# Kernel tuning notes

Hardware: AMD Instinct MI355X
Metric: run time of the kernel (lower is better)

The kernel has to match this reference:

```python
import jax, jax.numpy as jnp
import numpy as np

KSIZE = 3
PAD = (KSIZE - 1) // 2
SIGMA = 0.15 * KSIZE + 0.35  # 0.8, used for BOTH spatial and range weights (as in source)


def gaussian_kernel(ksize, sigma):
    if sigma <= 0:
        sigma = 0.3 * ((ksize - 1) * 0.5 - 1) + 0.8
    xs = np.arange(ksize, dtype=np.float32) - ksize // 2
    k1 = np.exp(-xs ** 2 / (2.0 * sigma ** 2))
    k = k1[:, None] * k1[None, :]
    return jnp.asarray((k / k.sum()).astype(np.float32))


def setup_inputs() -> dict:
    key = jax.random.key(0)
    ks = jax.random.split(key, 5)
    B, C_in, H, W = 8, 256, 128, 128
    C2 = 128
    x1 = jax.random.normal(ks[0], (B, C_in, H, W), jnp.float32)
    x2 = jax.random.normal(ks[1], (B, C2, 2 * H, 2 * W), jnp.float32)
    # Conv2d(in_ch, 1, kernel_size=1): weight [out=1, in], bias [1]
    w1 = jax.random.normal(ks[2], (1, C_in), jnp.float32) / np.float32(np.sqrt(C_in))
    b1 = jnp.zeros((1,), jnp.float32)
    # ConvTranspose2d(1, 1, k=2, s=2): weight [2, 2], bias [1]
    wt = jax.random.normal(ks[3], (2, 2), jnp.float32) * 0.5
    bt = jnp.zeros((1,), jnp.float32)
    return {"x1": x1, "x2": x2, "w1": w1, "b1": b1, "wt": wt, "bt": bt}


def reference(x1, x2, w1, b1, wt, bt):
    # 1x1 conv: [B, C_in, H, W] -> [B, 1, H, W]
    y = jnp.einsum('bchw,oc->bohw', x1, w1) + b1[None, :, None, None]
    B, _, H, W = y.shape
    # ConvTranspose2d(1,1,k=2,s=2): out[2h+dh, 2w+dw] = y[h,w] * wt[dh,dw] + bt
    up = (y[:, :, :, None, :, None] * wt[None, None, None, :, None, :]).reshape(
        B, 1, 2 * H, 2 * W) + bt[None, :, None, None]
    Hu, Wu = 2 * H, 2 * W
    # reflect pad then extract ksize x ksize patches (unfold equivalent)
    xp = jnp.pad(up, ((0, 0), (0, 0), (PAD, PAD), (PAD, PAD)), mode='reflect')
    patches = jnp.stack(
        [xp[:, :, i:i + Hu, j:j + Wu] for i in range(KSIZE) for j in range(KSIZE)],
        axis=-1)  # [B, 1, Hu, Wu, K*K]
    w_space = gaussian_kernel(KSIZE, SIGMA).reshape(-1)  # [K*K]
    diff = patches - up[..., None]
    w_color = jnp.exp(-(diff ** 2) / (2.0 * SIGMA ** 2))
    weights = w_color * w_space  # joint bilateral weights
    filtered = (weights * patches).sum(-1) / weights.sum(-1)  # [B, 1, Hu, Wu]
    gate = jax.nn.sigmoid(filtered)
    return gate * x2 + x2
```

## Files before the change

### kernel.cpp

```cpp
#include <hip/hip_runtime.h>
#include <hip/hip_bf16.h>


#define B     8
#define CIN   256
#define H     128
#define W     128
#define C2    128
#define HU    256
#define WU    256

__global__ __launch_bounds__(256) void conv1x1_kernel(
    const float* __restrict__ x1, const float* __restrict__ w1,
    const float* __restrict__ b1, float* __restrict__ y)
{
    __shared__ float wsh[CIN];
    int tid = threadIdx.x;
    wsh[tid] = w1[tid];
    __syncthreads();

    int t  = blockIdx.x * 256 + tid;
    int b  = t >> 14;
    int hw = t & 16383;

    const float* p = x1 + (size_t)b * CIN * H * W + hw;
    float acc = 0.f;
    #pragma unroll 8
    for (int c = 0; c < CIN; ++c)
        acc += p[(size_t)c * (H * W)] * wsh[c];
    y[t] = acc + b1[0];
}

__device__ __forceinline__ int refl(int i, int n) {
    return i < 0 ? -i : (i >= n ? 2 * n - 2 - i : i);
}

__global__ __launch_bounds__(256) void bilateral_gate_kernel(
    const float* __restrict__ y, const float* __restrict__ x2,
    const float* __restrict__ wt, const float* __restrict__ bt,
    float* __restrict__ out)
{
    int t   = blockIdx.x * 256 + threadIdx.x;
    int wq  = t & 63;
    int hu  = (t >> 6) & 255;
    int b   = t >> 14;
    int wu0 = wq * 4;

    const float* yb = y + (size_t)b * (H * W);
    float w2x2[4] = { wt[0], wt[1], wt[2], wt[3] };
    float btv = bt[0];

    float u[3][6];
    #pragma unroll
    for (int r = 0; r < 3; ++r) {
        int i  = refl(hu - 1 + r, HU);
        int iy = (i >> 1) * W;
        int ib = (i & 1) << 1;
        #pragma unroll
        for (int c = 0; c < 6; ++c) {
            int j = refl(wu0 - 1 + c, WU);
            u[r][c] = yb[iy + (j >> 1)] * w2x2[ib | (j & 1)] + btv;
        }
    }

    const float inv2s2 = 0.78125f;
    const float e1 = expf(-inv2s2);
    float k1v[3] = { e1, 1.f, e1 };

    float scale[4];
    #pragma unroll
    for (int p = 0; p < 4; ++p) {
        float ctr = u[1][p + 1];
        float num = 0.f, den = 0.f;
        #pragma unroll
        for (int r = 0; r < 3; ++r) {
            #pragma unroll
            for (int c = 0; c < 3; ++c) {
                float pv = u[r][p + c];
                float d  = pv - ctr;
                float w  = expf(-(d * d) * inv2s2) * (k1v[r] * k1v[c]);
                num += w * pv;
                den += w;
            }
        }
        float f = num / den;
        float g = 1.f / (1.f + expf(-f));
        scale[p] = 1.f + g;
    }

    size_t base = (size_t)b * C2 * HU * WU + (size_t)hu * WU + wu0;
    const float4* xp = (const float4*)(x2 + base);
    float4*       op = (float4*)(out + base);
    const int cstride = HU * WU / 4;

    #pragma unroll 4
    for (int c = 0; c < C2; ++c) {
        float4 v = xp[(size_t)c * cstride];
        v.x *= scale[0];
        v.y *= scale[1];
        v.z *= scale[2];
        v.w *= scale[3];
        op[(size_t)c * cstride] = v;
    }
}

extern "C" void kernel_launch(void* const* d_in, const int* in_sizes, int n_in,
                              void* d_out, int out_size, void* d_ws, size_t ws_size,
                              hipStream_t stream) {
    const float* x1 = (const float*)d_in[0];
    const float* x2 = (const float*)d_in[1];
    const float* w1 = (const float*)d_in[2];
    const float* b1 = (const float*)d_in[3];
    const float* wt = (const float*)d_in[4];
    const float* bt = (const float*)d_in[5];
    float* out = (float*)d_out;
    float* y   = (float*)d_ws;

    conv1x1_kernel<<<512, 256, 0, stream>>>(x1, w1, b1, y);
    bilateral_gate_kernel<<<512, 256, 0, stream>>>(y, x2, wt, bt, out);
}
```

Measured before the change: 527.0 us.

## Split channel loops across threads in conv and gate kernels for more parallelism

```diff
diff --git a/kernel.cpp b/kernel.cpp
--- a/kernel.cpp
+++ b/kernel.cpp
@@ -15,20 +15,43 @@
     const float* __restrict__ b1, float* __restrict__ y)
 {
     __shared__ float wsh[CIN];
+    __shared__ float4 sred[256];
     int tid = threadIdx.x;
     wsh[tid] = w1[tid];
     __syncthreads();
 
-    int t  = blockIdx.x * 256 + tid;
-    int b  = t >> 14;
-    int hw = t & 16383;
+    int b      = blockIdx.x >> 6;
+    int hwbase = (blockIdx.x & 63) * 256;
 
-    const float* p = x1 + (size_t)b * CIN * H * W + hw;
-    float acc = 0.f;
+    int q  = tid & 63;
+    int cc = tid >> 6;
+
+    const float4* p = (const float4*)(x1 + (size_t)b * CIN * H * W + hwbase) + q;
+    const int cstride = H * W / 4;
+
+    float4 acc = make_float4(0.f, 0.f, 0.f, 0.f);
+    int c0 = cc * 64;
     #pragma unroll 8
-    for (int c = 0; c < CIN; ++c)
-        acc += p[(size_t)c * (H * W)] * wsh[c];
-    y[t] = acc + b1[0];
+    for (int k = 0; k < 64; ++k) {
+        int c = c0 + k;
+        float4 v = p[(size_t)c * cstride];
+        float wv = wsh[c];
+        acc.x += v.x * wv; acc.y += v.y * wv;
+        acc.z += v.z * wv; acc.w += v.w * wv;
+    }
+    sred[tid] = acc;
+    __syncthreads();
+
+    if (cc == 0) {
+        float4 a = sred[q], b2 = sred[q + 64], c2 = sred[q + 128], d2 = sred[q + 192];
+        float bias = b1[0];
+        float4 r;
+        r.x = a.x + b2.x + c2.x + d2.x + bias;
+        r.y = a.y + b2.y + c2.y + d2.y + bias;
+        r.z = a.z + b2.z + c2.z + d2.z + bias;
+        r.w = a.w + b2.w + c2.w + d2.w + bias;
+        ((float4*)(y + (size_t)b * H * W + hwbase))[q] = r;
+    }
 }
 
 __device__ __forceinline__ int refl(int i, int n) {
@@ -40,43 +63,43 @@
     const float* __restrict__ wt, const float* __restrict__ bt,
     float* __restrict__ out)
 {
-    int t   = blockIdx.x * 256 + threadIdx.x;
-    int wq  = t & 63;
-    int hu  = (t >> 6) & 255;
-    int b   = t >> 14;
-    int wu0 = wq * 4;
+    __shared__ float scale_sh[WU];
 
-    const float* yb = y + (size_t)b * (H * W);
-    float w2x2[4] = { wt[0], wt[1], wt[2], wt[3] };
-    float btv = bt[0];
+    int hu = blockIdx.x & 255;
+    int b  = blockIdx.x >> 8;
+    int tid = threadIdx.x;
 
-    float u[3][6];
-    #pragma unroll
-    for (int r = 0; r < 3; ++r) {
-        int i  = refl(hu - 1 + r, HU);
-        int iy = (i >> 1) * W;
-        int ib = (i & 1) << 1;
+    {
+        int wu = tid;
+        const float* yb = y + (size_t)b * (H * W);
+        float w00 = wt[0], w01 = wt[1], w10 = wt[2], w11 = wt[3];
+        float btv = bt[0];
+
+        float u[3][3];
         #pragma unroll
-        for (int c = 0; c < 6; ++c) {
-            int j = refl(wu0 - 1 + c, WU);
-            u[r][c] = yb[iy + (j >> 1)] * w2x2[ib | (j & 1)] + btv;
+        for (int r = 0; r < 3; ++r) {
+            int i  = refl(hu - 1 + r, HU);
+            int iy = (i >> 1) * W;
+            float wr0 = (i & 1) ? w10 : w00;
+            float wr1 = (i & 1) ? w11 : w01;
+            #pragma unroll
+            for (int c = 0; c < 3; ++c) {
+                int j = refl(wu - 1 + c, WU);
+                u[r][c] = yb[iy + (j >> 1)] * ((j & 1) ? wr1 : wr0) + btv;
+            }
         }
-    }
 
-    const float inv2s2 = 0.78125f;
-    const float e1 = expf(-inv2s2);
-    float k1v[3] = { e1, 1.f, e1 };
+        const float inv2s2 = 0.78125f;
+        const float e1 = expf(-inv2s2);
+        float k1v[3] = { e1, 1.f, e1 };
 
-    float scale[4];
-    #pragma unroll
-    for (int p = 0; p < 4; ++p) {
-        float ctr = u[1][p + 1];
+        float ctr = u[1][1];
         float num = 0.f, den = 0.f;
         #pragma unroll
         for (int r = 0; r < 3; ++r) {
             #pragma unroll
             for (int c = 0; c < 3; ++c) {
-                float pv = u[r][p + c];
+                float pv = u[r][c];
                 float d  = pv - ctr;
                 float w  = expf(-(d * d) * inv2s2) * (k1v[r] * k1v[c]);
                 num += w * pv;
@@ -85,22 +108,24 @@
         }
         float f = num / den;
         float g = 1.f / (1.f + expf(-f));
-        scale[p] = 1.f + g;
+        scale_sh[wu] = 1.f + g;
     }
+    __syncthreads();
 
-    size_t base = (size_t)b * C2 * HU * WU + (size_t)hu * WU + wu0;
-    const float4* xp = (const float4*)(x2 + base);
-    float4*       op = (float4*)(out + base);
+    int g  = tid & 63;
+    int cc = tid >> 6;
+    float4 sc = ((const float4*)scale_sh)[g];
+
+    size_t base = (size_t)b * C2 * HU * WU + (size_t)hu * WU + (size_t)g * 4;
     const int cstride = HU * WU / 4;
+    const float4* xp = (const float4*)(x2 + base) + (size_t)(cc * 32) * cstride;
+    float4*       op = (float4*)(out + base)     + (size_t)(cc * 32) * cstride;
 
-    #pragma unroll 4
-    for (int c = 0; c < C2; ++c) {
-        float4 v = xp[(size_t)c * cstride];
-        v.x *= scale[0];
-        v.y *= scale[1];
-        v.z *= scale[2];
-        v.w *= scale[3];
-        op[(size_t)c * cstride] = v;
+    #pragma unroll 8
+    for (int k = 0; k < 32; ++k) {
+        float4 v = xp[(size_t)k * cstride];
+        v.x *= sc.x; v.y *= sc.y; v.z *= sc.z; v.w *= sc.w;
+        op[(size_t)k * cstride] = v;
     }
 }
 
@@ -117,5 +142,5 @@
     float* y   = (float*)d_ws;
 
     conv1x1_kernel<<<512, 256, 0, stream>>>(x1, w1, b1, y);
-    bilateral_gate_kernel<<<512, 256, 0, stream>>>(y, x2, wt, bt, out);
+    bilateral_gate_kernel<<<B * HU, 256, 0, stream>>>(y, x2, wt, bt, out);
 }
```

After: 524.1 us. Within noise of the previous version (-0.5%).
